# Optimization experiments

Measured on AMD Instinct MI355X. Metric: run time of the kernel, lower is better.

Reference implementation:

```python
import jax, jax.numpy as jnp
import numpy as np

B, T, F = 2048, 24, 16
N = 65536
D = T * F


def setup_inputs() -> dict:
    key = jax.random.key(0)
    k1, k2, k3 = jax.random.split(key, 3)
    x = jax.random.normal(k1, (B, T, F), dtype=jnp.float32)
    X_train = jax.random.normal(k2, (N, D), dtype=jnp.float32)
    Y_train = jax.random.normal(k3, (N, 24, 1), dtype=jnp.float32)
    return {"x": x, "X_train": X_train, "Y_train": Y_train}


def reference(x, X_train, Y_train):
    x_flat = x.reshape(x.shape[0], -1)  # [B, D]
    # Euclidean cdist via ||a||^2 + ||b||^2 - 2 a.b (GEMM-dominated)
    xx = jnp.sum(x_flat * x_flat, axis=1, keepdims=True)       # [B, 1]
    tt = jnp.sum(X_train * X_train, axis=1)[None, :]           # [1, N]
    cross = x_flat @ X_train.T                                  # [B, N]
    d2 = jnp.maximum(xx + tt - 2.0 * cross, 0.0)
    distances = jnp.sqrt(d2)                                    # [B, N]
    nearest = jnp.argmin(distances, axis=1)                     # [B]
    y_pred = Y_train[nearest]                                   # [B, 24, 1]
    return y_pred
```

## Files before the change

### kernel.cpp

```cpp
#include <hip/hip_runtime.h>
#include <cfloat>

#define B_Q 2048
#define N_T 65536
#define DIM 384
#define NSTRIPS 32
#define TILES 8
#define KSTEPS 12
#define TOTAL_STEPS (TILES * KSTEPS)

typedef __attribute__((ext_vector_type(8))) _Float16 f16x8;
typedef __attribute__((ext_vector_type(4))) float f32x4;

__global__ void split_kernel(const float* __restrict__ in, _Float16* __restrict__ hi,
                             _Float16* __restrict__ lo, int n8) {
  int i = blockIdx.x * 256 + threadIdx.x;
  if (i >= n8) return;
  float4 a = ((const float4*)in)[2 * i];
  float4 b = ((const float4*)in)[2 * i + 1];
  float v[8] = {a.x, a.y, a.z, a.w, b.x, b.y, b.z, b.w};
  f16x8 h, l;
#pragma unroll
  for (int j = 0; j < 8; ++j) {
    _Float16 hj = (_Float16)v[j];
    h[j] = hj;
    l[j] = (_Float16)(v[j] - (float)hj);
  }
  *(f16x8*)(hi + 8 * (size_t)i) = h;
  *(f16x8*)(lo + 8 * (size_t)i) = l;
}

__global__ void tt_kernel(const float* __restrict__ Xt, float* __restrict__ tt) {
  const int wave = threadIdx.x >> 6;
  const int lane = threadIdx.x & 63;
  const int row = blockIdx.x * 4 + wave;
  const float* p = Xt + (size_t)row * DIM;
  float s = 0.f;
#pragma unroll
  for (int i = 0; i < DIM / 64; ++i) {
    float v = p[lane + 64 * i];
    s = fmaf(v, v, s);
  }
#pragma unroll
  for (int off = 32; off > 0; off >>= 1) s += __shfl_xor(s, off, 64);
  if (lane == 0) tt[row] = s;
}

__global__ __launch_bounds__(512, 2) void dist_mfma2(
    const _Float16* __restrict__ xh, const _Float16* __restrict__ xl,
    const _Float16* __restrict__ th, const _Float16* __restrict__ tl,
    const float* __restrict__ tt, float* __restrict__ pval, int* __restrict__ pidx) {
  __shared__ __align__(16) char SM[65536];
  const int AH = 0, AL = 16384, BH = 32768, BL = 49152;

  const int t = threadIdx.x;
  const int lane = t & 63;
  const int wid = t >> 6;
  const int wm = wid >> 1, wn = wid & 1;
  const int r15 = lane & 15, g = lane >> 4;
  const int qbase = blockIdx.y * 256;
  const int strip = blockIdx.x;

  const int r0 = t >> 2, ch = t & 3;
  const int sch = ch ^ ((r0 >> 1) & 3);
  const int wo = r0 * 64 + sch * 16;
  const size_t aoff = (size_t)(qbase + r0) * DIM + ch * 8;
  const size_t boff = (size_t)(strip * 2048 + r0) * DIM + ch * 8;

  f16x8 sreg[8];
  auto stage_load = [&](int step) {
    int tile = step / KSTEPS;
    int kt = step - tile * KSTEPS;
    size_t a0 = aoff + kt * 32;
    size_t b0 = boff + (size_t)tile * (256 * DIM) + kt * 32;
    sreg[0] = *(const f16x8*)(xh + a0);
    sreg[1] = *(const f16x8*)(xh + a0 + (size_t)128 * DIM);
    sreg[2] = *(const f16x8*)(xl + a0);
    sreg[3] = *(const f16x8*)(xl + a0 + (size_t)128 * DIM);
    sreg[4] = *(const f16x8*)(th + b0);
    sreg[5] = *(const f16x8*)(th + b0 + (size_t)128 * DIM);
    sreg[6] = *(const f16x8*)(tl + b0);
    sreg[7] = *(const f16x8*)(tl + b0 + (size_t)128 * DIM);
  };
  auto stage_write = [&]() {
    *(f16x8*)(SM + AH + wo) = sreg[0];
    *(f16x8*)(SM + AH + wo + 8192) = sreg[1];
    *(f16x8*)(SM + AL + wo) = sreg[2];
    *(f16x8*)(SM + AL + wo + 8192) = sreg[3];
    *(f16x8*)(SM + BH + wo) = sreg[4];
    *(f16x8*)(SM + BH + wo + 8192) = sreg[5];
    *(f16x8*)(SM + BL + wo) = sreg[6];
    *(f16x8*)(SM + BL + wo + 8192) = sreg[7];
  };
  auto frag = [&](int base, int row, int gg) -> f16x8 {
    int off = base + row * 64 + ((gg ^ ((row >> 1) & 3)) << 4);
    return *(const f16x8*)(SM + off);
  };

  f32x4 acc[4][8];
#pragma unroll
  for (int mf = 0; mf < 4; ++mf)
#pragma unroll
    for (int nf = 0; nf < 8; ++nf) acc[mf][nf] = (f32x4){0.f, 0.f, 0.f, 0.f};

  float bestv = FLT_MAX;
  int besti = 0x7fffffff;

  stage_load(0);
  stage_write();
  __syncthreads();

  for (int step = 0; step < TOTAL_STEPS; ++step) {
    const int tile = step / KSTEPS;
    const int kt = step - tile * KSTEPS;
    const bool has_next = (step + 1 < TOTAL_STEPS);
    if (has_next) stage_load(step + 1);

    f16x8 ah[4], al[4];
#pragma unroll
    for (int mf = 0; mf < 4; ++mf) {
      int row = wm * 64 + mf * 16 + r15;
      ah[mf] = frag(AH, row, g);
      al[mf] = frag(AL, row, g);
    }
#pragma unroll
    for (int nf = 0; nf < 8; ++nf) {
      int row = wn * 128 + nf * 16 + r15;
      f16x8 bh = frag(BH, row, g);
      f16x8 bl = frag(BL, row, g);
#pragma unroll
      for (int mf = 0; mf < 4; ++mf) {
        acc[mf][nf] = __builtin_amdgcn_mfma_f32_16x16x32_f16(ah[mf], bh, acc[mf][nf], 0, 0, 0);
        acc[mf][nf] = __builtin_amdgcn_mfma_f32_16x16x32_f16(ah[mf], bl, acc[mf][nf], 0, 0, 0);
        acc[mf][nf] = __builtin_amdgcn_mfma_f32_16x16x32_f16(al[mf], bh, acc[mf][nf], 0, 0, 0);
      }
    }

    if (kt == KSTEPS - 1) {
      const int nb = strip * 2048 + tile * 256;
      float ttv[8];
#pragma unroll
      for (int nf = 0; nf < 8; ++nf) ttv[nf] = tt[nb + wn * 128 + nf * 16 + r15];
#pragma unroll
      for (int mf = 0; mf < 4; ++mf)
#pragma unroll
        for (int j = 0; j < 4; ++j) {
          float v = fmaf(-2.f, acc[mf][0][j], ttv[0]);
          int ix = nb + wn * 128 + r15;
#pragma unroll
          for (int nf = 1; nf < 8; ++nf) {
            float s = fmaf(-2.f, acc[mf][nf][j], ttv[nf]);
            if (s < v) { v = s; ix = nb + wn * 128 + nf * 16 + r15; }
          }
#pragma unroll
          for (int off = 1; off < 16; off <<= 1) {
            float ov = __shfl_xor(v, off, 64);
            int oi = __shfl_xor(ix, off, 64);
            if (ov < v || (ov == v && oi < ix)) { v = ov; ix = oi; }
          }
          float rv = __shfl(v, ((lane >> 2) & 3) << 4, 64);
          int ri = __shfl(ix, ((lane >> 2) & 3) << 4, 64);
          if ((lane >> 4) == mf && (lane & 3) == j) {
            if (rv < bestv || (rv == bestv && ri < besti)) { bestv = rv; besti = ri; }
          }
        }
#pragma unroll
      for (int mf = 0; mf < 4; ++mf)
#pragma unroll
        for (int nf = 0; nf < 8; ++nf) acc[mf][nf] = (f32x4){0.f, 0.f, 0.f, 0.f};
    }

    __syncthreads();
    if (has_next) {
      stage_write();
      __syncthreads();
    }
  }

  const int q = qbase + wm * 64 + lane;
  pval[(size_t)q * 64 + strip * 2 + wn] = bestv;
  pidx[(size_t)q * 64 + strip * 2 + wn] = besti;
}

__global__ void reduce64(const float* __restrict__ pval, const int* __restrict__ pidx,
                         const float* __restrict__ Y, float* __restrict__ out) {
  const int wid = threadIdx.x >> 6;
  const int lane = threadIdx.x & 63;
  const int q = blockIdx.x * 4 + wid;
  float v = pval[(size_t)q * 64 + lane];
  int ix = pidx[(size_t)q * 64 + lane];
#pragma unroll
  for (int off = 32; off > 0; off >>= 1) {
    float ov = __shfl_xor(v, off, 64);
    int oi = __shfl_xor(ix, off, 64);
    if (ov < v || (ov == v && oi < ix)) { v = ov; ix = oi; }
  }
  if (lane < 24) out[(size_t)q * 24 + lane] = Y[(size_t)ix * 24 + lane];
}

#define BK 16
#define PAD 132
__global__ __launch_bounds__(256) void dist_f32(
    const float* __restrict__ x, const float* __restrict__ Xt,
    const float* __restrict__ tt, float* __restrict__ pval, int* __restrict__ pidx) {
  __shared__ float As[BK][PAD];
  __shared__ float Bs[BK][PAD];
  const int t = threadIdx.x;
  const int tx = t & 15;
  const int ty = t >> 4;
  const int qbase = blockIdx.x * 128;
  const int strip = blockIdx.y;
  float bestv[8];
  int besti[8];
#pragma unroll
  for (int i = 0; i < 8; ++i) { bestv[i] = FLT_MAX; besti[i] = 0x7fffffff; }
  for (int tile = 0; tile < 8; ++tile) {
    const int nbase = strip * 1024 + tile * 128;
    float acc[8][8];
#pragma unroll
    for (int i = 0; i < 8; ++i)
#pragma unroll
      for (int j = 0; j < 8; ++j) acc[i][j] = 0.f;
    for (int kt = 0; kt < DIM / BK; ++kt) {
      const int kbase = kt * BK;
      __syncthreads();
#pragma unroll
      for (int it = 0; it < 2; ++it) {
        int idx = t + it * 256;
        int row = idx >> 2;
        int k4 = (idx & 3) << 2;
        float4 va = *(const float4*)(x + (size_t)(qbase + row) * DIM + kbase + k4);
        As[k4 + 0][row] = va.x; As[k4 + 1][row] = va.y;
        As[k4 + 2][row] = va.z; As[k4 + 3][row] = va.w;
        float4 vb = *(const float4*)(Xt + (size_t)(nbase + row) * DIM + kbase + k4);
        Bs[k4 + 0][row] = vb.x; Bs[k4 + 1][row] = vb.y;
        Bs[k4 + 2][row] = vb.z; Bs[k4 + 3][row] = vb.w;
      }
      __syncthreads();
#pragma unroll
      for (int kk = 0; kk < BK; ++kk) {
        float4 a0 = *(const float4*)&As[kk][ty * 4];
        float4 a1 = *(const float4*)&As[kk][64 + ty * 4];
        float4 b0 = *(const float4*)&Bs[kk][tx * 4];
        float4 b1 = *(const float4*)&Bs[kk][64 + tx * 4];
        float a[8] = {a0.x, a0.y, a0.z, a0.w, a1.x, a1.y, a1.z, a1.w};
        float b[8] = {b0.x, b0.y, b0.z, b0.w, b1.x, b1.y, b1.z, b1.w};
#pragma unroll
        for (int i = 0; i < 8; ++i)
#pragma unroll
          for (int j = 0; j < 8; ++j) acc[i][j] = fmaf(a[i], b[j], acc[i][j]);
      }
    }
    int cols[8];
    float ttv[8];
#pragma unroll
    for (int j = 0; j < 8; ++j) {
      cols[j] = nbase + (j < 4 ? tx * 4 + j : 64 + tx * 4 + (j - 4));
      ttv[j] = tt[cols[j]];
    }
#pragma unroll
    for (int i = 0; i < 8; ++i)
#pragma unroll
      for (int j = 0; j < 8; ++j) {
        float s = fmaf(-2.f, acc[i][j], ttv[j]);
        if (s < bestv[i] || (s == bestv[i] && cols[j] < besti[i])) {
          bestv[i] = s; besti[i] = cols[j];
        }
      }
  }
#pragma unroll
  for (int i = 0; i < 8; ++i) {
    float v = bestv[i];
    int ix = besti[i];
#pragma unroll
    for (int off = 1; off < 16; off <<= 1) {
      float ov = __shfl_xor(v, off, 64);
      int oi = __shfl_xor(ix, off, 64);
      if (ov < v || (ov == v && oi < ix)) { v = ov; ix = oi; }
    }
    if (tx == 0) {
      int row = qbase + (i < 4 ? ty * 4 + i : 64 + ty * 4 + (i - 4));
      pval[(size_t)row * 64 + strip] = v;
      pidx[(size_t)row * 64 + strip] = ix;
    }
  }
}

extern "C" void kernel_launch(void* const* d_in, const int* in_sizes, int n_in,
                              void* d_out, int out_size, void* d_ws, size_t ws_size,
                              hipStream_t stream) {
  const float* x  = (const float*)d_in[0];
  const float* Xt = (const float*)d_in[1];
  const float* Y  = (const float*)d_in[2];
  float* out = (float*)d_out;

  _Float16* th = (_Float16*)d_ws;
  _Float16* tl = th + (size_t)N_T * DIM;
  _Float16* xh = tl + (size_t)N_T * DIM;
  _Float16* xl = xh + (size_t)B_Q * DIM;
  float* tt = (float*)(xl + (size_t)B_Q * DIM);
  float* pval = tt + N_T;
  int* pidx = (int*)(pval + (size_t)B_Q * 64);
  size_t need = (size_t)((char*)(pidx + (size_t)B_Q * 64) - (char*)d_ws);

  if (ws_size >= need) {
    split_kernel<<<(N_T * DIM / 8 + 255) / 256, 256, 0, stream>>>(Xt, th, tl, N_T * DIM / 8);
    split_kernel<<<(B_Q * DIM / 8 + 255) / 256, 256, 0, stream>>>(x, xh, xl, B_Q * DIM / 8);
    tt_kernel<<<N_T / 4, 256, 0, stream>>>(Xt, tt);
    dist_mfma2<<<dim3(NSTRIPS, B_Q / 256), 512, 0, stream>>>(xh, xl, th, tl, tt, pval, pidx);
    reduce64<<<B_Q / 4, 256, 0, stream>>>(pval, pidx, Y, out);
  } else {
    float* tt2 = (float*)d_ws;
    float* pv2 = tt2 + N_T;
    int* pi2 = (int*)(pv2 + (size_t)B_Q * 64);
    tt_kernel<<<N_T / 4, 256, 0, stream>>>(Xt, tt2);
    dist_f32<<<dim3(B_Q / 128, 64), 256, 0, stream>>>(x, Xt, tt2, pv2, pi2);
    reduce64<<<B_Q / 4, 256, 0, stream>>>(pv2, pi2, Y, out);
  }
}
```

Before: 484.8 us.

## Pre-tile split operands and stream B tiles into LDS with direct loads

The split kernels now emit the hi/lo fp16 images of X_train and x in a tile-major, pre-swizzled layout, so each K-step's B tile is one contiguous 32KB block. The distance kernel copies that block global-to-LDS with global_load_lds into a double buffer, dropping the register staging and one barrier per step. A fragments are read straight from global memory (L2/cache) instead of being staged in LDS. The risks are uncoalesced strided reads in the split kernels and extra global latency on the A fragment loads inside the MFMA loop.

```diff
diff --git a/kernel.cpp b/kernel.cpp
--- a/kernel.cpp
+++ b/kernel.cpp
@@ -12,22 +12,57 @@
 typedef __attribute__((ext_vector_type(8))) _Float16 f16x8;
 typedef __attribute__((ext_vector_type(4))) float f32x4;
 
-__global__ void split_kernel(const float* __restrict__ in, _Float16* __restrict__ hi,
-                             _Float16* __restrict__ lo, int n8) {
-  int i = blockIdx.x * 256 + threadIdx.x;
-  if (i >= n8) return;
-  float4 a = ((const float4*)in)[2 * i];
-  float4 b = ((const float4*)in)[2 * i + 1];
-  float v[8] = {a.x, a.y, a.z, a.w, b.x, b.y, b.z, b.w};
+__device__ __forceinline__ void gload16(const void* g, void* l) {
+  __builtin_amdgcn_global_load_lds(
+      (const __attribute__((address_space(1))) void*)g,
+      (__attribute__((address_space(3))) void*)l, 16, 0, 0);
+}
+
+__global__ void splitA_kernel(const float* __restrict__ x, _Float16* __restrict__ Aimg) {
+  int gid = blockIdx.x * 256 + threadIdx.x;
+  int chunk = gid & 3;
+  int r1 = gid >> 2;
+  int row = r1 & 255;
+  int r2 = r1 >> 8;
+  int kt = r2 % 12;
+  int qb = r2 / 12;
+  const float* src = x + (size_t)(qb * 256 + row) * DIM + kt * 32 + chunk * 8;
   f16x8 h, l;
 #pragma unroll
   for (int j = 0; j < 8; ++j) {
-    _Float16 hj = (_Float16)v[j];
+    float v = src[j];
+    _Float16 hj = (_Float16)v;
     h[j] = hj;
-    l[j] = (_Float16)(v[j] - (float)hj);
-  }
-  *(f16x8*)(hi + 8 * (size_t)i) = h;
-  *(f16x8*)(lo + 8 * (size_t)i) = l;
+    l[j] = (_Float16)(v - (float)hj);
+  }
+  size_t base = ((size_t)(qb * 12 + kt) * 2) * 8192 + row * 32 + chunk * 8;
+  *(f16x8*)(Aimg + base) = h;
+  *(f16x8*)(Aimg + base + 8192) = l;
+}
+
+__global__ void splitB_kernel(const float* __restrict__ Xt, _Float16* __restrict__ Bimg) {
+  int gid = blockIdx.x * 256 + threadIdx.x;
+  int t = gid & 511;
+  int r1 = gid >> 9;
+  int rb = r1 & 1;
+  int r2 = r1 >> 1;
+  int kt = r2 % 12;
+  int tileg = r2 / 12;
+  int r0 = t >> 2;
+  int c = (t & 3) ^ ((r0 >> 1) & 3);
+  int row = tileg * 256 + rb * 128 + r0;
+  const float* src = Xt + (size_t)row * DIM + kt * 32 + c * 8;
+  f16x8 h, l;
+#pragma unroll
+  for (int j = 0; j < 8; ++j) {
+    float v = src[j];
+    _Float16 hj = (_Float16)v;
+    h[j] = hj;
+    l[j] = (_Float16)(v - (float)hj);
+  }
+  size_t base = ((size_t)(tileg * 12 + kt) * 4 + rb) * 4096 + t * 8;
+  *(f16x8*)(Bimg + base) = h;
+  *(f16x8*)(Bimg + base + 8192) = l;
 }
 
 __global__ void tt_kernel(const float* __restrict__ Xt, float* __restrict__ tt) {
@@ -46,56 +81,21 @@
   if (lane == 0) tt[row] = s;
 }
 
-__global__ __launch_bounds__(512, 2) void dist_mfma2(
-    const _Float16* __restrict__ xh, const _Float16* __restrict__ xl,
-    const _Float16* __restrict__ th, const _Float16* __restrict__ tl,
+__global__ __launch_bounds__(512, 2) void dist_mfma3(
+    const char* __restrict__ Aimg, const char* __restrict__ Bimg,
     const float* __restrict__ tt, float* __restrict__ pval, int* __restrict__ pidx) {
-  __shared__ __align__(16) char SM[65536];
-  const int AH = 0, AL = 16384, BH = 32768, BL = 49152;
+  __shared__ __align__(16) char SM[2][32768];
 
   const int t = threadIdx.x;
   const int lane = t & 63;
   const int wid = t >> 6;
   const int wm = wid >> 1, wn = wid & 1;
   const int r15 = lane & 15, g = lane >> 4;
-  const int qbase = blockIdx.y * 256;
   const int strip = blockIdx.x;
-
-  const int r0 = t >> 2, ch = t & 3;
-  const int sch = ch ^ ((r0 >> 1) & 3);
-  const int wo = r0 * 64 + sch * 16;
-  const size_t aoff = (size_t)(qbase + r0) * DIM + ch * 8;
-  const size_t boff = (size_t)(strip * 2048 + r0) * DIM + ch * 8;
-
-  f16x8 sreg[8];
-  auto stage_load = [&](int step) {
-    int tile = step / KSTEPS;
-    int kt = step - tile * KSTEPS;
-    size_t a0 = aoff + kt * 32;
-    size_t b0 = boff + (size_t)tile * (256 * DIM) + kt * 32;
-    sreg[0] = *(const f16x8*)(xh + a0);
-    sreg[1] = *(const f16x8*)(xh + a0 + (size_t)128 * DIM);
-    sreg[2] = *(const f16x8*)(xl + a0);
-    sreg[3] = *(const f16x8*)(xl + a0 + (size_t)128 * DIM);
-    sreg[4] = *(const f16x8*)(th + b0);
-    sreg[5] = *(const f16x8*)(th + b0 + (size_t)128 * DIM);
-    sreg[6] = *(const f16x8*)(tl + b0);
-    sreg[7] = *(const f16x8*)(tl + b0 + (size_t)128 * DIM);
-  };
-  auto stage_write = [&]() {
-    *(f16x8*)(SM + AH + wo) = sreg[0];
-    *(f16x8*)(SM + AH + wo + 8192) = sreg[1];
-    *(f16x8*)(SM + AL + wo) = sreg[2];
-    *(f16x8*)(SM + AL + wo + 8192) = sreg[3];
-    *(f16x8*)(SM + BH + wo) = sreg[4];
-    *(f16x8*)(SM + BH + wo + 8192) = sreg[5];
-    *(f16x8*)(SM + BL + wo) = sreg[6];
-    *(f16x8*)(SM + BL + wo + 8192) = sreg[7];
-  };
-  auto frag = [&](int base, int row, int gg) -> f16x8 {
-    int off = base + row * 64 + ((gg ^ ((row >> 1) & 3)) << 4);
-    return *(const f16x8*)(SM + off);
-  };
+  const int qb = blockIdx.y;
+  const int qbase = qb * 256;
+
+  const int aoff = (wm * 64 + r15) * 64 + g * 16;
 
   f32x4 acc[4][8];
 #pragma unroll
@@ -106,28 +106,39 @@
   float bestv = FLT_MAX;
   int besti = 0x7fffffff;
 
-  stage_load(0);
-  stage_write();
-  __syncthreads();
-
-  for (int step = 0; step < TOTAL_STEPS; ++step) {
-    const int tile = step / KSTEPS;
-    const int kt = step - tile * KSTEPS;
-    const bool has_next = (step + 1 < TOTAL_STEPS);
-    if (has_next) stage_load(step + 1);
-
+  auto stageB = [&](int s, int buf) {
+    int tile = s / KSTEPS;
+    int kt = s - tile * KSTEPS;
+    const char* base = Bimg + ((size_t)((strip * 8 + tile) * 12 + kt) * 4) * 8192 + t * 16;
+    char* dst = &SM[buf][0] + t * 16;
+    gload16(base,         dst);
+    gload16(base + 8192,  dst + 8192);
+    gload16(base + 16384, dst + 16384);
+    gload16(base + 24576, dst + 24576);
+  };
+
+  stageB(0, 0);
+
+  for (int s = 0; s < TOTAL_STEPS; ++s) {
+    __syncthreads();
+    if (s + 1 < TOTAL_STEPS) stageB(s + 1, (s + 1) & 1);
+    const int tile = s / KSTEPS;
+    const int kt = s - tile * KSTEPS;
+    const char* buf = &SM[s & 1][0];
+
+    const char* ak = Aimg + ((size_t)(qb * 12 + kt)) * 32768;
     f16x8 ah[4], al[4];
 #pragma unroll
     for (int mf = 0; mf < 4; ++mf) {
-      int row = wm * 64 + mf * 16 + r15;
-      ah[mf] = frag(AH, row, g);
-      al[mf] = frag(AL, row, g);
+      ah[mf] = *(const f16x8*)(ak + aoff + mf * 1024);
+      al[mf] = *(const f16x8*)(ak + 16384 + aoff + mf * 1024);
     }
 #pragma unroll
     for (int nf = 0; nf < 8; ++nf) {
       int row = wn * 128 + nf * 16 + r15;
-      f16x8 bh = frag(BH, row, g);
-      f16x8 bl = frag(BL, row, g);
+      int boff = row * 64 + ((g ^ ((row >> 1) & 3)) << 4);
+      f16x8 bh = *(const f16x8*)(buf + boff);
+      f16x8 bl = *(const f16x8*)(buf + 16384 + boff);
 #pragma unroll
       for (int mf = 0; mf < 4; ++mf) {
         acc[mf][nf] = __builtin_amdgcn_mfma_f32_16x16x32_f16(ah[mf], bh, acc[mf][nf], 0, 0, 0);
@@ -149,8 +160,8 @@
           int ix = nb + wn * 128 + r15;
 #pragma unroll
           for (int nf = 1; nf < 8; ++nf) {
-            float s = fmaf(-2.f, acc[mf][nf][j], ttv[nf]);
-            if (s < v) { v = s; ix = nb + wn * 128 + nf * 16 + r15; }
+            float sv = fmaf(-2.f, acc[mf][nf][j], ttv[nf]);
+            if (sv < v) { v = sv; ix = nb + wn * 128 + nf * 16 + r15; }
           }
 #pragma unroll
           for (int off = 1; off < 16; off <<= 1) {
@@ -168,12 +179,6 @@
       for (int mf = 0; mf < 4; ++mf)
 #pragma unroll
         for (int nf = 0; nf < 8; ++nf) acc[mf][nf] = (f32x4){0.f, 0.f, 0.f, 0.f};
-    }
-
-    __syncthreads();
-    if (has_next) {
-      stage_write();
-      __syncthreads();
     }
   }
 
@@ -294,20 +299,20 @@
   const float* Y  = (const float*)d_in[2];
   float* out = (float*)d_out;
 
-  _Float16* th = (_Float16*)d_ws;
-  _Float16* tl = th + (size_t)N_T * DIM;
-  _Float16* xh = tl + (size_t)N_T * DIM;
-  _Float16* xl = xh + (size_t)B_Q * DIM;
-  float* tt = (float*)(xl + (size_t)B_Q * DIM);
+  char* Bimg = (char*)d_ws;
+  const size_t BIMG_BYTES = (size_t)256 * 12 * 4 * 8192;
+  char* Aimg = Bimg + BIMG_BYTES;
+  const size_t AIMG_BYTES = (size_t)8 * 12 * 2 * 16384;
+  float* tt = (float*)(Aimg + AIMG_BYTES);
   float* pval = tt + N_T;
   int* pidx = (int*)(pval + (size_t)B_Q * 64);
   size_t need = (size_t)((char*)(pidx + (size_t)B_Q * 64) - (char*)d_ws);
 
   if (ws_size >= need) {
-    split_kernel<<<(N_T * DIM / 8 + 255) / 256, 256, 0, stream>>>(Xt, th, tl, N_T * DIM / 8);
-    split_kernel<<<(B_Q * DIM / 8 + 255) / 256, 256, 0, stream>>>(x, xh, xl, B_Q * DIM / 8);
+    splitB_kernel<<<12288, 256, 0, stream>>>(Xt, (_Float16*)Bimg);
+    splitA_kernel<<<384, 256, 0, stream>>>(x, (_Float16*)Aimg);
     tt_kernel<<<N_T / 4, 256, 0, stream>>>(Xt, tt);
-    dist_mfma2<<<dim3(NSTRIPS, B_Q / 256), 512, 0, stream>>>(xh, xl, th, tl, tt, pval, pidx);
+    dist_mfma3<<<dim3(NSTRIPS, B_Q / 256), 512, 0, stream>>>(Aimg, Bimg, tt, pval, pidx);
     reduce64<<<B_Q / 4, 256, 0, stream>>>(pval, pidx, Y, out);
   } else {
     float* tt2 = (float*)d_ws;
```

Result: no change. 482.6 us (-0.5%).
